# Kernel tuning notes

Measured on AMD Instinct MI355X. Metric: run time of the kernel, lower is better.

The kernel has to match this reference:

```python
import jax, jax.numpy as jnp
import numpy as np

B, A, C, G = 8, 65536, 80, 16
TOPK = 50            # pre_anchor_topk
VAR0, VAR1 = 0.1, 0.2  # cfg['variance']
BBOX_T = 0.5
GAMMA = 2.0
ALPHA = 0.5
SL1_W, SL1_BETA = 0.75, 0.11


@jax.custom_vjp
def st_clip(x):
    # Clip.apply: clamp fwd, straight-through bwd
    return jnp.clip(x, 1e-12, None)

def _st_fwd(x):
    return jnp.clip(x, 1e-12, None), None

def _st_bwd(_, g):
    return (g,)

st_clip.defvjp(_st_fwd, _st_bwd)


def point_form(b):  # (cx,cy,w,h) -> (x1,y1,x2,y2)
    return jnp.concatenate([b[..., :2] - b[..., 2:] * 0.5,
                            b[..., :2] + b[..., 2:] * 0.5], axis=-1)


def decode(loc, priors):  # returns center form
    cxcy = priors[..., :2] + loc[..., :2] * VAR0 * priors[..., 2:]
    wh = priors[..., 2:] * jnp.exp(loc[..., 2:] * VAR1)
    return jnp.concatenate([cxcy, wh], axis=-1)


def encode(matched, priors):  # matched: point form, priors: center form
    g_cxcy = ((matched[..., :2] + matched[..., 2:]) * 0.5 - priors[..., :2]) / (VAR0 * priors[..., 2:])
    g_wh = jnp.log((matched[..., 2:] - matched[..., :2]) / priors[..., 2:]) / VAR1
    return jnp.concatenate([g_cxcy, g_wh], axis=-1)


def jaccard(a, b):  # a: [G,4], b: [A,4], point form -> [G,A] IoU
    lt = jnp.maximum(a[:, None, :2], b[None, :, :2])
    rb = jnp.minimum(a[:, None, 2:], b[None, :, 2:])
    wh = jnp.clip(rb - lt, 0.0, None)
    inter = wh[..., 0] * wh[..., 1]
    area_a = (a[:, 2] - a[:, 0]) * (a[:, 3] - a[:, 1])
    area_b = (b[:, 2] - b[:, 0]) * (b[:, 3] - b[:, 1])
    return inter / (area_a[:, None] + area_b[None, :] - inter)


def positive_bag_loss(logits):  # logits: [G, K], bag over K
    w = 1.0 / st_clip(1.0 - logits)
    w = w / jnp.sum(w, axis=1, keepdims=True)
    bag = jnp.sum(w * logits, axis=1)
    return -jnp.log(bag)


def setup_inputs() -> dict:
    key = jax.random.key(0)
    k1, k2, k3, k4, k5, k6 = jax.random.split(key, 6)
    box_regression = jax.random.normal(k1, (B, A, 4), jnp.float32) * 0.1
    cls_logits = jax.random.normal(k2, (B, A, C), jnp.float32) - 2.0
    a_cxcy = jax.random.uniform(k3, (A, 2), jnp.float32, 0.1, 0.9)
    a_wh = jax.random.uniform(k4, (A, 2), jnp.float32, 0.05, 0.3)
    anchors = jnp.concatenate([a_cxcy, a_wh], axis=-1)  # center form
    t_cxcy = jax.random.uniform(k5, (B, G, 2), jnp.float32, 0.2, 0.8)
    t_wh = jax.random.uniform(k6, (B, G, 2), jnp.float32, 0.05, 0.3)
    targets_boxes = jnp.concatenate([t_cxcy - t_wh * 0.5, t_cxcy + t_wh * 0.5], axis=-1)  # point form
    labels = jax.random.randint(jax.random.fold_in(key, 7), (B, G), 0, C)
    return {"box_regression": box_regression, "cls_logits": cls_logits,
            "anchors": anchors, "targets_boxes": targets_boxes, "labels": labels}


def _per_image(box_reg, cls_p, anchors, tboxes, tlabels):
    # ---- box_prob branch (torch: set_grad_enabled(False)) ----
    box_loc = point_form(decode(box_reg, anchors))
    iou = jaccard(tboxes, box_loc)                                  # [G, A]
    t2 = jnp.clip(jnp.max(iou, axis=1, keepdims=True), BBOX_T + 1e-12, None)
    obp = jnp.clip((iou - BBOX_T) / (t2 - BBOX_T), 0.0, 1.0)        # [G, A]
    # sparse per-class scatter + per-class max over objects == segment_max over labels
    seg = jax.ops.segment_max(obp, tlabels, num_segments=C)         # [C, A]
    image_box_prob = jax.lax.stop_gradient(jnp.maximum(seg, 0.0).T)  # [A, C]

    # ---- positive (bag) branch ----
    mqm = jaccard(tboxes, point_form(anchors))                      # [G, A]
    _, matched = jax.lax.top_k(mqm, TOPK)                           # [G, K]
    matched_cls_prob = cls_p[matched, tlabels[:, None]]             # [G, K]
    mot = encode(tboxes[:, None, :], anchors[matched])              # [G, K, 4]
    val = mot - box_reg[matched]
    sl1 = jnp.where(jnp.abs(val) < SL1_BETA,
                    0.5 / SL1_BETA * val * val,
                    jnp.abs(val) - 0.5 * SL1_BETA)
    reg_loss = SL1_W * jnp.sum(sl1, axis=-1)                        # [G, K]
    matched_box_prob = jnp.exp(-reg_loss)
    pos = positive_bag_loss(matched_cls_prob * matched_box_prob)    # [G]
    return pos, image_box_prob


def reference(box_regression, cls_logits, anchors, targets_boxes, labels):
    cls_prob = jax.nn.sigmoid(cls_logits)
    pos, box_prob = jax.vmap(_per_image, in_axes=(0, 0, None, 0, 0))(
        box_regression, cls_prob, anchors, targets_boxes, labels)
    n_pos = B * G
    positive_loss = jnp.sum(pos) / max(1, n_pos)
    x = cls_prob * (1.0 - box_prob)                                 # [B, A, C]
    negative_loss = jnp.sum(x ** GAMMA * -jnp.log(1.0 - x)) / max(1, n_pos * TOPK)
    return positive_loss * ALPHA, negative_loss * (1.0 - ALPHA)
```

## Files before the change

kernel.cpp:

```cpp
#include <hip/hip_runtime.h>
#include <hip/hip_bf16.h>
#include <math.h>

#define BB 8
#define AA 65536
#define CC 80
#define GG 16
#define KK 50
#define NBG (BB*GG)
#define CAP 2048
#define BINS 64
#define NCH 128
#define CHUNK (AA/NCH)
#define NIOU (NCH*BB)
#define NNEG 4096

#define OFF_ACC   0
#define OFF_T2    16
#define OFF_THR   528
#define OFF_GMASK 1040
#define OFF_CNT   3600
#define OFF_CCNT  4112
#define OFF_HIST  4128
#define HEAD_WORDS 9224
#define HEAD0 1032
#define OFF_CANDV 36896
#define OFF_CANDI 1085472
#define OFF_CLIST 2134048

__global__ void k_pre(unsigned* __restrict__ w, const int* __restrict__ labels,
                      unsigned* __restrict__ gmask){
    int tid=threadIdx.x;
    if (blockIdx.x==0){
        for (int i=tid; i<HEAD0; i+=256) w[i]=0u;
        __syncthreads();
        if (tid<NBG){
            int b=tid>>4; int c=labels[tid];
            atomicOr(&gmask[b*CC+c], 1u<<(tid&15));
        }
    } else {
        for (unsigned i=HEAD0+(blockIdx.x-1)*256u+tid; i<HEAD_WORDS; i+=63u*256u) w[i]=0u;
    }
}

__global__ __launch_bounds__(256) void k_iou_neg(const float4* __restrict__ anc4,
        const float4* __restrict__ reg4, const float4* __restrict__ tgt4,
        const float4* __restrict__ lg4,
        unsigned* __restrict__ t2u, unsigned* __restrict__ ghist,
        int* __restrict__ ccnt, unsigned* __restrict__ clist,
        double* __restrict__ acc){
    __shared__ unsigned hist[GG][BINS];
    __shared__ float4 stb[GG];
    __shared__ float sarea[GG];
    __shared__ unsigned st2[GG];
    __shared__ unsigned lbuf[CHUNK];
    __shared__ int lcnt, lbase;
    __shared__ double wsum[4];
    int tid=threadIdx.x;
    int x=blockIdx.x;

    if (x>=NIOU){
        double loc=0.0;
        const unsigned n4=(unsigned)BB*AA*CC/4u;
        for (unsigned i=(unsigned)(x-NIOU)*256u+tid; i<n4; i+=(unsigned)NNEG*256u){
            float4 v=lg4[i];
            float l[4]={v.x,v.y,v.z,v.w};
            float fs=0.f;
            #pragma unroll
            for (int k=0; k<4; ++k){
                float e=__expf(l[k]);
                float s=e*__builtin_amdgcn_rcpf(1.f+e);
                fs+=s*s*__logf(1.f+e);
            }
            loc+=(double)fs;
        }
        for (int off=32; off; off>>=1) loc+=__shfl_down(loc,off);
        if ((tid&63)==0) wsum[tid>>6]=loc;
        __syncthreads();
        if (tid==0) atomicAdd(&acc[1],wsum[0]+wsum[1]+wsum[2]+wsum[3]);
        return;
    }

    int blk=x&(NCH-1), b=x>>7;
    for (int j=tid; j<GG*BINS; j+=256) ((unsigned*)hist)[j]=0u;
    if (tid<GG){
        float4 tb=tgt4[b*GG+tid];
        stb[tid]=tb;
        sarea[tid]=(tb.z-tb.x)*(tb.w-tb.y);
        st2[tid]=0u;
    }
    if (tid==0) lcnt=0;
    __syncthreads();
    float mx[GG];
    #pragma unroll
    for (int g=0; g<GG; ++g) mx[g]=0.f;
    int abase=blk*CHUNK+tid;
    for (int it=0; it<CHUNK/256; ++it){
        int a=abase+it*256;
        float4 an=anc4[a];
        float4 br=reg4[b*AA+a];
        float dcx=an.x+br.x*0.1f*an.z;
        float dcy=an.y+br.y*0.1f*an.w;
        float dw=an.z*__expf(br.z*0.2f);
        float dh=an.w*__expf(br.w*0.2f);
        float dx1=dcx-dw*0.5f, dy1=dcy-dh*0.5f, dx2=dcx+dw*0.5f, dy2=dcy+dh*0.5f;
        float dA=dw*dh;
        float ax1=an.x-an.z*0.5f, ay1=an.y-an.w*0.5f;
        float ax2=an.x+an.z*0.5f, ay2=an.y+an.w*0.5f;
        float aA=an.z*an.w;
        bool emit=false;
        #pragma unroll
        for (int g=0; g<GG; ++g){
            float4 tb=stb[g];
            float tA=sarea[g];
            {
                float lx=fmaxf(tb.x,dx1), ly=fmaxf(tb.y,dy1);
                float rx=fminf(tb.z,dx2), ry=fminf(tb.w,dy2);
                float w_=rx-lx, h_=ry-ly;
                if (w_>0.f && h_>0.f){
                    float inter=w_*h_;
                    float iou=inter/(tA+dA-inter);
                    mx[g]=fmaxf(mx[g],iou);
                    if (iou>0.5f) emit=true;
                }
            }
            {
                float lx=fmaxf(tb.x,ax1), ly=fmaxf(tb.y,ay1);
                float rx=fminf(tb.z,ax2), ry=fminf(tb.w,ay2);
                float w_=rx-lx, h_=ry-ly;
                if (w_>0.f && h_>0.f){
                    float inter=w_*h_;
                    float m=inter/(tA+aA-inter);
                    int bin=min(BINS-1,(int)(m*(float)BINS));
                    atomicAdd(&hist[g][bin],1u);
                }
            }
        }
        if (emit){
            int p=atomicAdd(&lcnt,1);
            lbuf[p]=(unsigned)a;
        }
    }
    #pragma unroll
    for (int g=0; g<GG; ++g){
        float v=mx[g];
        for (int off=32; off; off>>=1) v=fmaxf(v,__shfl_down(v,off));
        if ((tid&63)==0) atomicMax(&st2[g],__float_as_uint(v));
    }
    __syncthreads();
    if (tid<GG) atomicMax(&t2u[b*GG+tid],st2[tid]);
    if (tid==0 && lcnt>0) lbase=atomicAdd(ccnt,lcnt);
    __syncthreads();
    for (int j=tid; j<GG*BINS; j+=256){
        unsigned v=((unsigned*)hist)[j];
        if (v) atomicAdd(&ghist[b*GG*BINS+j],v);
    }
    unsigned bb=(unsigned)b<<16;
    for (int j=tid; j<lcnt; j+=256) clist[lbase+j]=bb|lbuf[j];
}

__global__ __launch_bounds__(256) void k_candthr(const float4* __restrict__ anc4,
        const float4* __restrict__ tgt4, const unsigned* __restrict__ ghist,
        int* __restrict__ gcnt, float* __restrict__ candv, int* __restrict__ candi){
    __shared__ unsigned hist[GG][BINS];
    __shared__ float4 stb[GG];
    __shared__ float sarea[GG];
    __shared__ float sthr[GG];
    int tid=threadIdx.x, blk=blockIdx.x, b=blockIdx.y;
    int lane=tid&63, wv=tid>>6;
    for (int j=tid; j<GG*BINS; j+=256) ((unsigned*)hist)[j]=ghist[b*GG*BINS+j];
    if (tid<GG){
        float4 tb=tgt4[b*GG+tid];
        stb[tid]=tb;
        sarea[tid]=(tb.z-tb.x)*(tb.w-tb.y);
    }
    __syncthreads();
    #pragma unroll
    for (int gg=0; gg<4; ++gg){
        int g=wv*4+gg;
        unsigned v=hist[g][lane];
        #pragma unroll
        for (int off=1; off<64; off<<=1){
            unsigned o=__shfl_down(v,off);
            if (lane+off<64) v+=o;
        }
        unsigned long long mask=__ballot(v>=KK);
        int bs = mask ? (63-__clzll(mask)) : 0;
        if (lane==0) sthr[g]=(float)bs;
    }
    __syncthreads();
    int abase=blk*CHUNK+tid;
    for (int it=0; it<CHUNK/256; ++it){
        int a=abase+it*256;
        float4 an=anc4[a];
        float ax1=an.x-an.z*0.5f, ay1=an.y-an.w*0.5f;
        float ax2=an.x+an.z*0.5f, ay2=an.y+an.w*0.5f;
        float aA=an.z*an.w;
        #pragma unroll
        for (int g=0; g<GG; ++g){
            float4 tb=stb[g];
            float m=0.f;
            {
                float lx=fmaxf(tb.x,ax1), ly=fmaxf(tb.y,ay1);
                float rx=fminf(tb.z,ax2), ry=fminf(tb.w,ay2);
                float w_=rx-lx, h_=ry-ly;
                if (w_>0.f && h_>0.f){
                    float inter=w_*h_;
                    m=inter/(sarea[g]+aA-inter);
                }
            }
            bool push=(m>0.f && m*(float)BINS>=sthr[g]);
            unsigned long long msk=__ballot(push);
            if (msk){
                int bg=b*GG+g;
                int n=__popcll(msk);
                int ldr=__ffsll((long long)msk)-1;
                int base=0;
                if (lane==ldr) base=atomicAdd(&gcnt[bg],n);
                base=__shfl(base,ldr);
                if (push){
                    int p=base+(int)__popcll(msk&((1ull<<lane)-1ull));
                    if (p<CAP){ candv[bg*CAP+p]=m; candi[bg*CAP+p]=a; }
                }
            }
        }
    }
}

__global__ __launch_bounds__(256) void k_selcorr(const float4* __restrict__ anc4,
        const float4* __restrict__ reg4, const float4* __restrict__ tgt4,
        const float* __restrict__ logits, const int* __restrict__ labels,
        const int* __restrict__ gcnt, const float* __restrict__ candv,
        const int* __restrict__ candi, const unsigned* __restrict__ gmask,
        const float* __restrict__ t2f, const int* __restrict__ ccnt,
        const unsigned* __restrict__ clist, double* __restrict__ acc){
    __shared__ float cv[CAP];
    __shared__ int ci[CAP];
    __shared__ double wsum[4];
    int tid=threadIdx.x;
    int x=blockIdx.x;

    if (x>=NBG){
        int n=*ccnt;
        double loc=0.0;
        for (int i=(x-NBG)*256+tid; i<n; i+=256*256){
            unsigned key=clist[i];
            int b=key>>16, a=key&0xffff;
            float4 an=anc4[a];
            float4 br=reg4[b*AA+a];
            float dcx=an.x+br.x*0.1f*an.z;
            float dcy=an.y+br.y*0.1f*an.w;
            float dw=an.z*__expf(br.z*0.2f);
            float dh=an.w*__expf(br.w*0.2f);
            float dx1=dcx-dw*0.5f, dy1=dcy-dh*0.5f, dx2=dcx+dw*0.5f, dy2=dcy+dh*0.5f;
            float dA=dw*dh;
            float obp[GG];
            #pragma unroll
            for (int g=0; g<GG; ++g){
                float4 tb=tgt4[b*GG+g];
                float lx=fmaxf(tb.x,dx1), ly=fmaxf(tb.y,dy1);
                float rx=fminf(tb.z,dx2), ry=fminf(tb.w,dy2);
                float w_=fmaxf(rx-lx,0.f), h_=fmaxf(ry-ly,0.f);
                float inter=w_*h_;
                float tA=(tb.z-tb.x)*(tb.w-tb.y);
                float iou=inter/(tA+dA-inter);
                float d=t2f[b*GG+g]-0.5f;
                float inv=(d>0.f)?1.f/d:0.f;
                obp[g]=fminf(fmaxf((iou-0.5f)*inv,0.f),1.f);
            }
            for (int c=0; c<CC; ++c){
                unsigned m=gmask[b*CC+c];
                if (!m) continue;
                float bp=0.f;
                while (m){ unsigned g=(unsigned)__builtin_ctz(m); m&=m-1u; bp=fmaxf(bp,obp[g]); }
                if (bp<=0.f) continue;
                float lg=logits[((size_t)b*AA+(size_t)a)*CC+c];
                float e=__expf(lg);
                float s=e*__builtin_amdgcn_rcpf(1.f+e);
                float xx=s*(1.f-bp);
                float fx=xx*xx*(-__logf(fmaxf(1.f-xx,1e-12f)));
                float fs=s*s*__logf(1.f+e);
                loc+=(double)(fx-fs);
            }
        }
        for (int off=32; off; off>>=1) loc+=__shfl_down(loc,off);
        if ((tid&63)==0) wsum[tid>>6]=loc;
        __syncthreads();
        if (tid==0) atomicAdd(&acc[1],wsum[0]+wsum[1]+wsum[2]+wsum[3]);
        return;
    }

    int bg=x; int b=bg>>4;
    int cnt=gcnt[bg]; if (cnt>CAP) cnt=CAP;
    for (int j=tid; j<cnt; j+=256){ cv[j]=candv[bg*CAP+j]; ci[j]=candi[bg*CAP+j]; }
    __syncthreads();
    if (tid>=64) return;
    int lane=tid;
    int myA=-1;
    for (int k=0; k<KK; ++k){
        float bv=-1e30f; int bi=0x7fffffff; int bj=-1;
        for (int j=lane; j<cnt; j+=64){
            float v=cv[j]; int ii=ci[j];
            if (v>bv || (v==bv && ii<bi)){ bv=v; bi=ii; bj=j; }
        }
        for (int off=32; off; off>>=1){
            float ov=__shfl_down(bv,off); int oi=__shfl_down(bi,off); int oj=__shfl_down(bj,off);
            if (ov>bv || (ov==bv && oi<bi)){ bv=ov; bi=oi; bj=oj; }
        }
        int wj=__shfl(bj,0); int wi=__shfl(bi,0); float wv=__shfl(bv,0);
        if (wv>-1e29f){
            if (lane==(wj&63)) cv[wj]=-1e30f;
            if (lane==k) myA=wi;
        }
    }
    float p=0.f, u=0.f;
    if (lane<KK && myA>=0){
        float4 tb=tgt4[bg];
        int a=myA;
        float4 an=anc4[a];
        int lab=labels[bg];
        float lg=logits[((size_t)b*AA+(size_t)a)*CC+lab];
        float mcp=1.f/(1.f+expf(-lg));
        float gcx=((tb.x+tb.z)*0.5f-an.x)/(0.1f*an.z);
        float gcy=((tb.y+tb.w)*0.5f-an.y)/(0.1f*an.w);
        float gw=logf((tb.z-tb.x)/an.z)/0.2f;
        float gh=logf((tb.w-tb.y)/an.w)/0.2f;
        float4 br=reg4[b*AA+a];
        float v0=gcx-br.x, v1=gcy-br.y, v2=gw-br.z, v3=gh-br.w;
        float s=0.f;
        {float av=fabsf(v0); s+=(av<0.11f)?4.545454545454546f*v0*v0:av-0.055f;}
        {float av=fabsf(v1); s+=(av<0.11f)?4.545454545454546f*v1*v1:av-0.055f;}
        {float av=fabsf(v2); s+=(av<0.11f)?4.545454545454546f*v2*v2:av-0.055f;}
        {float av=fabsf(v3); s+=(av<0.11f)?4.545454545454546f*v3*v3:av-0.055f;}
        float mbp=expf(-(0.75f*s));
        p=mcp*mbp;
        u=1.f/fmaxf(1.f-p,1e-12f);
    }
    float su=u, sp=u*p;
    for (int off=32; off; off>>=1){ su+=__shfl_down(su,off); sp+=__shfl_down(sp,off); }
    if (lane==0) atomicAdd(&acc[0],(double)(-logf(sp/su)));
}

__global__ void k_fin(const double* __restrict__ acc, float* __restrict__ out){
    out[0]=(float)(0.5*acc[0]/128.0);
    out[1]=(float)(0.5*acc[1]/6400.0);
}

extern "C" void kernel_launch(void* const* d_in, const int* in_sizes, int n_in,
                              void* d_out, int out_size, void* d_ws, size_t ws_size,
                              hipStream_t stream){
    const float4* reg4=(const float4*)d_in[0];
    const float*  logits=(const float*)d_in[1];
    const float4* anc4=(const float4*)d_in[2];
    const float4* tgt4=(const float4*)d_in[3];
    const int*    labels=(const int*)d_in[4];
    char* ws=(char*)d_ws;
    double*   acc   =(double*)(ws+OFF_ACC);
    float*    t2f   =(float*)(ws+OFF_T2);
    unsigned* gmask =(unsigned*)(ws+OFF_GMASK);
    int*      gcnt  =(int*)(ws+OFF_CNT);
    int*      ccnt  =(int*)(ws+OFF_CCNT);
    unsigned* ghist =(unsigned*)(ws+OFF_HIST);
    float*    candv =(float*)(ws+OFF_CANDV);
    int*      candi =(int*)(ws+OFF_CANDI);
    unsigned* clist =(unsigned*)(ws+OFF_CLIST);

    k_pre<<<64,256,0,stream>>>((unsigned*)ws,labels,gmask);
    k_iou_neg<<<NIOU+NNEG,256,0,stream>>>(anc4,reg4,tgt4,(const float4*)logits,
                                          (unsigned*)t2f,ghist,ccnt,clist,acc);
    k_candthr<<<dim3(NCH,BB),256,0,stream>>>(anc4,tgt4,ghist,gcnt,candv,candi);
    k_selcorr<<<NBG+256,256,0,stream>>>(anc4,reg4,tgt4,logits,labels,gcnt,candv,candi,
                                        gmask,t2f,ccnt,clist,acc);
    k_fin<<<1,1,0,stream>>>(acc,(float*)d_out);
}
```

Before: 342.7 us.

## Reorder neg-loss blocks first, halve their count, unroll loads for more memory parallelism

The negative-loss blocks now occupy the low block indices, so they are scheduled before the IoU blocks, and their count is halved. Each block's grid-stride loop is replaced by a fixed five-iteration loop that issues four independent float4 loads per iteration to raise memory-level parallelism. The kernel also gets a launch-bounds occupancy hint of 8 blocks per CU. The fixed trip count assumes the logits size divides exactly into 2048*256*20 float4s, and the occupancy hint may limit registers for the IoU path.

```diff
diff --git a/kernel.cpp b/kernel.cpp
--- a/kernel.cpp
+++ b/kernel.cpp
@@ -13,7 +13,7 @@
 #define NCH 128
 #define CHUNK (AA/NCH)
 #define NIOU (NCH*BB)
-#define NNEG 4096
+#define NNEG 2048
 
 #define OFF_ACC   0
 #define OFF_T2    16
@@ -43,7 +43,7 @@
     }
 }
 
-__global__ __launch_bounds__(256) void k_iou_neg(const float4* __restrict__ anc4,
+__global__ __launch_bounds__(256,8) void k_iou_neg(const float4* __restrict__ anc4,
         const float4* __restrict__ reg4, const float4* __restrict__ tgt4,
         const float4* __restrict__ lg4,
         unsigned* __restrict__ t2u, unsigned* __restrict__ ghist,
@@ -59,19 +59,31 @@
     int tid=threadIdx.x;
     int x=blockIdx.x;
 
-    if (x>=NIOU){
+    if (x<NNEG){
         double loc=0.0;
-        const unsigned n4=(unsigned)BB*AA*CC/4u;
-        for (unsigned i=(unsigned)(x-NIOU)*256u+tid; i<n4; i+=(unsigned)NNEG*256u){
-            float4 v=lg4[i];
-            float l[4]={v.x,v.y,v.z,v.w};
+        unsigned i0=(unsigned)x*256u+(unsigned)tid;
+        const unsigned S=(unsigned)NNEG*256u;
+        #pragma unroll
+        for (int gp=0; gp<5; ++gp){
+            float4 v0=lg4[i0];
+            float4 v1=lg4[i0+S];
+            float4 v2=lg4[i0+2u*S];
+            float4 v3=lg4[i0+3u*S];
+            i0+=4u*S;
             float fs=0.f;
-            #pragma unroll
-            for (int k=0; k<4; ++k){
-                float e=__expf(l[k]);
-                float s=e*__builtin_amdgcn_rcpf(1.f+e);
-                fs+=s*s*__logf(1.f+e);
-            }
+            #define NEGF4(v) { \
+                float l0=v.x,l1=v.y,l2=v.z,l3=v.w; \
+                float e0=__expf(l0), e1=__expf(l1), e2=__expf(l2), e3=__expf(l3); \
+                float s0=e0*__builtin_amdgcn_rcpf(1.f+e0); \
+                float s1=e1*__builtin_amdgcn_rcpf(1.f+e1); \
+                float s2=e2*__builtin_amdgcn_rcpf(1.f+e2); \
+                float s3=e3*__builtin_amdgcn_rcpf(1.f+e3); \
+                fs+=s0*s0*__logf(1.f+e0); \
+                fs+=s1*s1*__logf(1.f+e1); \
+                fs+=s2*s2*__logf(1.f+e2); \
+                fs+=s3*s3*__logf(1.f+e3); }
+            NEGF4(v0) NEGF4(v1) NEGF4(v2) NEGF4(v3)
+            #undef NEGF4
             loc+=(double)fs;
         }
         for (int off=32; off; off>>=1) loc+=__shfl_down(loc,off);
@@ -81,7 +93,8 @@
         return;
     }
 
-    int blk=x&(NCH-1), b=x>>7;
+    int xx=x-NNEG;
+    int blk=xx&(NCH-1), b=xx>>7;
     for (int j=tid; j<GG*BINS; j+=256) ((unsigned*)hist)[j]=0u;
     if (tid<GG){
         float4 tb=tgt4[b*GG+tid];
@@ -366,7 +379,7 @@
     unsigned* clist =(unsigned*)(ws+OFF_CLIST);
 
     k_pre<<<64,256,0,stream>>>((unsigned*)ws,labels,gmask);
-    k_iou_neg<<<NIOU+NNEG,256,0,stream>>>(anc4,reg4,tgt4,(const float4*)logits,
+    k_iou_neg<<<NNEG+NIOU,256,0,stream>>>(anc4,reg4,tgt4,(const float4*)logits,
                                           (unsigned*)t2f,ghist,ccnt,clist,acc);
     k_candthr<<<dim3(NCH,BB),256,0,stream>>>(anc4,tgt4,ghist,gcnt,candv,candi);
     k_selcorr<<<NBG+256,256,0,stream>>>(anc4,reg4,tgt4,logits,labels,gcnt,candv,candi,
```

After: 704.5 us. 106% more time.
